# Performance work log

Hardware: AMD Instinct MI355X
Metric: run time of the kernel (lower is better)

The kernel has to match this reference:

```python
import jax, jax.numpy as jnp
import numpy as np

B, N, C, T = 8, 4096, 8, 256


def setup_inputs() -> dict:
    key = jax.random.key(0)
    ks = jax.random.split(key, 5)
    x = jax.random.normal(ks[0], (B, N, C, T), dtype=jnp.float32)
    u1 = jax.random.normal(ks[1], (N,), dtype=jnp.float32) * (1.0 / np.sqrt(N))
    u2 = jax.random.normal(ks[2], (C, N), dtype=jnp.float32) * (1.0 / np.sqrt(C))
    u3 = jax.random.normal(ks[3], (C,), dtype=jnp.float32) * (1.0 / np.sqrt(C))
    b = jnp.zeros((1, T, T), dtype=jnp.float32)
    v = jax.random.normal(ks[4], (T, T), dtype=jnp.float32) * (1.0 / np.sqrt(T))
    return {"x": x, "u1": u1, "u2": u2, "u3": u3, "b": b, "v": v}


def reference(x, u1, u2, u3, b, v):
    # x: (B, N, C, T)
    # x_u1 = squeeze(dot(permute(x,(0,3,2,1)), u1)) -> (B, T, C)
    x_u1 = jnp.einsum('bnct,n->btc', x, u1)
    # lhs = x_u1 @ u2 -> (B, T, N)
    lhs = jnp.einsum('btc,cn->btn', x_u1, u2)
    # rhs = squeeze(dot(permute(x,(0,1,3,2)), u3)) -> (B, N, T)
    rhs = jnp.einsum('bnct,c->bnt', x, u3)
    # product = batch_dot(lhs, rhs) -> (B, T, T)
    product = jnp.einsum('btn,bns->bts', lhs, rhs)
    # E[b,i,j] = sum_k v[i,k] * sigmoid(product + b)[b,k,j]
    E = jnp.einsum('ik,bkj->bij', v, jax.nn.sigmoid(product + b))
    # hand-rolled stable softmax over last axis == jax.nn.softmax
    return jax.nn.softmax(E, axis=-1)
```

## Files before the change

### kernel.cpp

```cpp
#include <hip/hip_runtime.h>
#include <math.h>

#define B_ 8
#define N_ 4096
#define C_ 8
#define T_ 256
#define NCHUNK 32
#define CHUNKS (N_ / NCHUNK)

__global__ __launch_bounds__(256) void pass1(
    const float* __restrict__ x, const float* __restrict__ u1,
    const float* __restrict__ u2, const float* __restrict__ u3,
    float* __restrict__ p1, float* __restrict__ p2) {
  const int blk = blockIdx.x;
  const int b = blk / CHUNKS;
  const int chunk = blk % CHUNKS;
  const int n0 = chunk * NCHUNK;
  const int tid = threadIdx.x;
  const int sub = tid >> 6;
  const int lane = tid & 63;
  const int t0 = lane << 2;

  float u3r[C_];
#pragma unroll
  for (int c = 0; c < C_; ++c) u3r[c] = u3[c];

  float a1[C_][4];
  float a2[C_][4];
#pragma unroll
  for (int c = 0; c < C_; ++c)
#pragma unroll
    for (int q = 0; q < 4; ++q) { a1[c][q] = 0.f; a2[c][q] = 0.f; }

  for (int r = 0; r < NCHUNK / 4; ++r) {
    const int n = n0 + r * 4 + sub;
    const float* xp = x + ((size_t)(b * N_ + n) * C_) * T_ + t0;
    const float w1 = u1[n];
    float rh0 = 0.f, rh1 = 0.f, rh2 = 0.f, rh3 = 0.f;
#pragma unroll
    for (int c = 0; c < C_; ++c) {
      const float4 xv = *(const float4*)(xp + c * T_);
      rh0 = fmaf(u3r[c], xv.x, rh0);
      rh1 = fmaf(u3r[c], xv.y, rh1);
      rh2 = fmaf(u3r[c], xv.z, rh2);
      rh3 = fmaf(u3r[c], xv.w, rh3);
      a1[c][0] = fmaf(w1, xv.x, a1[c][0]);
      a1[c][1] = fmaf(w1, xv.y, a1[c][1]);
      a1[c][2] = fmaf(w1, xv.z, a1[c][2]);
      a1[c][3] = fmaf(w1, xv.w, a1[c][3]);
    }
#pragma unroll
    for (int c = 0; c < C_; ++c) {
      const float w2 = u2[c * N_ + n];
      a2[c][0] = fmaf(w2, rh0, a2[c][0]);
      a2[c][1] = fmaf(w2, rh1, a2[c][1]);
      a2[c][2] = fmaf(w2, rh2, a2[c][2]);
      a2[c][3] = fmaf(w2, rh3, a2[c][3]);
    }
  }

  __shared__ float red[4][C_ * T_];
  const size_t pbase = (size_t)blk * (C_ * T_);

#pragma unroll
  for (int c = 0; c < C_; ++c)
#pragma unroll
    for (int q = 0; q < 4; ++q) red[sub][c * T_ + t0 + q] = a1[c][q];
  __syncthreads();
  for (int e = tid; e < C_ * T_; e += 256)
    p1[pbase + e] = red[0][e] + red[1][e] + red[2][e] + red[3][e];
  __syncthreads();

#pragma unroll
  for (int c = 0; c < C_; ++c)
#pragma unroll
    for (int q = 0; q < 4; ++q) red[sub][c * T_ + t0 + q] = a2[c][q];
  __syncthreads();
  for (int e = tid; e < C_ * T_; e += 256)
    p2[pbase + e] = red[0][e] + red[1][e] + red[2][e] + red[3][e];
}

__global__ __launch_bounds__(256) void reduce2(
    const float* __restrict__ p1, const float* __restrict__ p2,
    float* __restrict__ x_u1, float* __restrict__ r2) {
  const int arr = blockIdx.x >> 8;
  const int g = (blockIdx.x & 255) >> 2;
  const int s = blockIdx.x & 3;
  const int idx = g * 256 + threadIdx.x;
  const int b = idx >> 11;
  const int e = idx & 2047;
  const float* src = arr ? p2 : p1;
  float* dst = arr ? r2 : x_u1;
  const float* q = src + (size_t)(b * CHUNKS + s * 32) * 2048 + e;
  float acc = 0.f;
#pragma unroll 8
  for (int k = 0; k < 32; ++k) acc += q[(size_t)k * 2048];
  atomicAdd(dst + idx, acc);
}

__global__ __launch_bounds__(256) void prodsig(
    const float* __restrict__ x_u1, const float* __restrict__ r2,
    const float* __restrict__ bias, float* __restrict__ S) {
  const int b = blockIdx.x >> 8;
  const int t = blockIdx.x & 255;
  const int j = threadIdx.x;
  float acc = bias[t * T_ + j];
#pragma unroll
  for (int c = 0; c < C_; ++c)
    acc = fmaf(x_u1[b * 2048 + c * T_ + t], r2[b * 2048 + c * T_ + j], acc);
  S[(size_t)blockIdx.x * T_ + j] = 1.f / (1.f + expf(-acc));
}

__global__ __launch_bounds__(256) void esoftmax(
    const float* __restrict__ v, const float* __restrict__ S,
    float* __restrict__ out) {
  __shared__ float vlds[8][T_];
  __shared__ float elds[8][T_];
  __shared__ float rmax[8], rinv[8];
  const int b = blockIdx.x >> 5;
  const int i0 = (blockIdx.x & 31) << 3;
  const int j = threadIdx.x;

#pragma unroll
  for (int r = 0; r < 8; ++r) vlds[r][j] = v[(i0 + r) * T_ + j];
  __syncthreads();

  float acc[8] = {0.f, 0.f, 0.f, 0.f, 0.f, 0.f, 0.f, 0.f};
  const float* Sb = S + (size_t)b * T_ * T_;
  for (int k = 0; k < T_; k += 4) {
    const float s0 = Sb[(k + 0) * T_ + j];
    const float s1 = Sb[(k + 1) * T_ + j];
    const float s2 = Sb[(k + 2) * T_ + j];
    const float s3 = Sb[(k + 3) * T_ + j];
#pragma unroll
    for (int r = 0; r < 8; ++r) {
      const float4 vv = *(const float4*)&vlds[r][k];
      acc[r] = fmaf(vv.x, s0,
               fmaf(vv.y, s1, fmaf(vv.z, s2, fmaf(vv.w, s3, acc[r]))));
    }
  }

#pragma unroll
  for (int r = 0; r < 8; ++r) elds[r][j] = acc[r];
  __syncthreads();

  const int wave = j >> 6, lane = j & 63;
  for (int r = wave; r < 8; r += 4) {
    float m = -INFINITY;
#pragma unroll
    for (int q = 0; q < 4; ++q) m = fmaxf(m, elds[r][lane + q * 64]);
#pragma unroll
    for (int off = 32; off > 0; off >>= 1) m = fmaxf(m, __shfl_xor(m, off, 64));
    float sm = 0.f;
#pragma unroll
    for (int q = 0; q < 4; ++q) sm += expf(elds[r][lane + q * 64] - m);
#pragma unroll
    for (int off = 32; off > 0; off >>= 1) sm += __shfl_xor(sm, off, 64);
    if (lane == 0) { rmax[r] = m; rinv[r] = 1.f / sm; }
  }
  __syncthreads();

  float* ob = out + ((size_t)b * T_ + i0) * T_;
#pragma unroll
  for (int r = 0; r < 8; ++r)
    ob[r * T_ + j] = expf(elds[r][j] - rmax[r]) * rinv[r];
}

extern "C" void kernel_launch(void* const* d_in, const int* in_sizes, int n_in,
                              void* d_out, int out_size, void* d_ws, size_t ws_size,
                              hipStream_t stream) {
  const float* x    = (const float*)d_in[0];
  const float* u1   = (const float*)d_in[1];
  const float* u2   = (const float*)d_in[2];
  const float* u3   = (const float*)d_in[3];
  const float* bias = (const float*)d_in[4];
  const float* v    = (const float*)d_in[5];
  float* out = (float*)d_out;

  char* ws = (char*)d_ws;
  float* p1   = (float*)(ws);
  float* p2   = (float*)(ws + (8u << 20));
  float* x_u1 = (float*)(ws + (16u << 20));
  float* r2   = (float*)(ws + (16u << 20) + (64u << 10));
  float* S    = (float*)(ws + (16u << 20) + (128u << 10));

  hipMemsetAsync(x_u1, 0, 128u << 10, stream);

  pass1<<<B_ * CHUNKS, 256, 0, stream>>>(x, u1, u2, u3, p1, p2);
  reduce2<<<512, 256, 0, stream>>>(p1, p2, x_u1, r2);
  prodsig<<<B_ * T_, 256, 0, stream>>>(x_u1, r2, bias, S);
  esoftmax<<<B_ * (T_ / 8), 256, 0, stream>>>(v, S, out);
}
```

Before: 385.6 us.

## Fuse product-sigmoid into E/softmax kernel and double pass1 chunk size

Removes the separate prodsig kernel and the intermediate S buffer, recomputing the rank-8 product and sigmoid inside the E/softmax kernel for each k. Each of the 32 blocks per batch now recomputes the full sigmoid matrix, which adds compute but saves the S write and read and one launch. The pass1 chunk size doubles, halving the number of partial-sum blocks and partial traffic, with reduce2 loop bounds adjusted to match. The fewer pass1 blocks (1024 to 512) may reduce parallelism on the dominant x-streaming pass.

```diff
diff --git a/kernel.cpp b/kernel.cpp
--- a/kernel.cpp
+++ b/kernel.cpp
@@ -5,7 +5,7 @@
 #define N_ 4096
 #define C_ 8
 #define T_ 256
-#define NCHUNK 32
+#define NCHUNK 64
 #define CHUNKS (N_ / NCHUNK)
 
 __global__ __launch_bounds__(256) void pass1(
@@ -91,28 +91,16 @@
   const int e = idx & 2047;
   const float* src = arr ? p2 : p1;
   float* dst = arr ? r2 : x_u1;
-  const float* q = src + (size_t)(b * CHUNKS + s * 32) * 2048 + e;
+  const float* q = src + (size_t)(b * CHUNKS + s * 16) * 2048 + e;
   float acc = 0.f;
 #pragma unroll 8
-  for (int k = 0; k < 32; ++k) acc += q[(size_t)k * 2048];
+  for (int k = 0; k < 16; ++k) acc += q[(size_t)k * 2048];
   atomicAdd(dst + idx, acc);
 }
 
-__global__ __launch_bounds__(256) void prodsig(
+__global__ __launch_bounds__(256) void pse(
     const float* __restrict__ x_u1, const float* __restrict__ r2,
-    const float* __restrict__ bias, float* __restrict__ S) {
-  const int b = blockIdx.x >> 8;
-  const int t = blockIdx.x & 255;
-  const int j = threadIdx.x;
-  float acc = bias[t * T_ + j];
-#pragma unroll
-  for (int c = 0; c < C_; ++c)
-    acc = fmaf(x_u1[b * 2048 + c * T_ + t], r2[b * 2048 + c * T_ + j], acc);
-  S[(size_t)blockIdx.x * T_ + j] = 1.f / (1.f + expf(-acc));
-}
-
-__global__ __launch_bounds__(256) void esoftmax(
-    const float* __restrict__ v, const float* __restrict__ S,
+    const float* __restrict__ bias, const float* __restrict__ v,
     float* __restrict__ out) {
   __shared__ float vlds[8][T_];
   __shared__ float elds[8][T_];
@@ -125,19 +113,20 @@
   for (int r = 0; r < 8; ++r) vlds[r][j] = v[(i0 + r) * T_ + j];
   __syncthreads();
 
+  float r2c[C_];
+#pragma unroll
+  for (int c = 0; c < C_; ++c) r2c[c] = r2[b * 2048 + c * T_ + j];
+  const float* xu = x_u1 + b * 2048;
+
   float acc[8] = {0.f, 0.f, 0.f, 0.f, 0.f, 0.f, 0.f, 0.f};
-  const float* Sb = S + (size_t)b * T_ * T_;
-  for (int k = 0; k < T_; k += 4) {
-    const float s0 = Sb[(k + 0) * T_ + j];
-    const float s1 = Sb[(k + 1) * T_ + j];
-    const float s2 = Sb[(k + 2) * T_ + j];
-    const float s3 = Sb[(k + 3) * T_ + j];
+#pragma unroll 4
+  for (int k = 0; k < T_; ++k) {
+    float p = bias[k * T_ + j];
 #pragma unroll
-    for (int r = 0; r < 8; ++r) {
-      const float4 vv = *(const float4*)&vlds[r][k];
-      acc[r] = fmaf(vv.x, s0,
-               fmaf(vv.y, s1, fmaf(vv.z, s2, fmaf(vv.w, s3, acc[r]))));
-    }
+    for (int c = 0; c < C_; ++c) p = fmaf(xu[c * T_ + k], r2c[c], p);
+    const float sg = 1.f / (1.f + __expf(-p));
+#pragma unroll
+    for (int r = 0; r < 8; ++r) acc[r] = fmaf(vlds[r][k], sg, acc[r]);
   }
 
 #pragma unroll
@@ -179,15 +168,13 @@
 
   char* ws = (char*)d_ws;
   float* p1   = (float*)(ws);
-  float* p2   = (float*)(ws + (8u << 20));
-  float* x_u1 = (float*)(ws + (16u << 20));
-  float* r2   = (float*)(ws + (16u << 20) + (64u << 10));
-  float* S    = (float*)(ws + (16u << 20) + (128u << 10));
+  float* p2   = (float*)(ws + (4u << 20));
+  float* x_u1 = (float*)(ws + (8u << 20));
+  float* r2   = (float*)(ws + (8u << 20) + (64u << 10));
 
   hipMemsetAsync(x_u1, 0, 128u << 10, stream);
 
   pass1<<<B_ * CHUNKS, 256, 0, stream>>>(x, u1, u2, u3, p1, p2);
   reduce2<<<512, 256, 0, stream>>>(p1, p2, x_u1, r2);
-  prodsig<<<B_ * T_, 256, 0, stream>>>(x_u1, r2, bias, S);
-  esoftmax<<<B_ * (T_ / 8), 256, 0, stream>>>(v, S, out);
+  pse<<<B_ * (T_ / 8), 256, 0, stream>>>(x_u1, r2, bias, v, out);
 }
```

After: 432.0 us. 12.0% more time.
